# Performance work log

Measured on AMD Instinct MI355X. Metric: run time of the kernel, lower is better.

## Reference

```python
import jax, jax.numpy as jnp
import numpy as np

B, S, D = 1, 2048, 4096
H, KV, HD = 32, 8, 128
REP = H // KV            # 4, GQA repeat factor
THETA = 500000.0
NEG = -1e9               # stand-in for -inf in additive causal mask


def _rope(x, cos, sin):
    # x: [B,S,h,HD]; complex rotation on interleaved (even,odd) pairs,
    # matching torch.view_as_complex on [..., HD/2, 2]
    xr, xi = x[..., 0::2], x[..., 1::2]
    c = cos[None, :, None, :]
    s = sin[None, :, None, :]
    out_r = xr * c - xi * s
    out_i = xr * s + xi * c
    return jnp.stack([out_r, out_i], axis=-1).reshape(x.shape)


def setup_inputs() -> dict:
    key = jax.random.key(0)
    ks = jax.random.split(key, 6)
    x = jax.random.normal(ks[0], (B, S, D), dtype=jnp.float32)
    # torch nn.Linear weights are [out, in]
    sc = 1.0 / np.sqrt(D)
    wq = jax.random.normal(ks[1], (H * HD, D), dtype=jnp.float32) * sc
    wk = jax.random.normal(ks[2], (KV * HD, D), dtype=jnp.float32) * sc
    wv = jax.random.normal(ks[3], (KV * HD, D), dtype=jnp.float32) * sc
    wo = jax.random.normal(ks[4], (D, H * HD), dtype=jnp.float32) * sc
    # RoPE freqs_cis = exp(i * t * theta_f), stored as cos/sin [S, HD/2]
    freqs = 1.0 / (THETA ** (jnp.arange(0, HD, 2, dtype=jnp.float32) / HD))
    ang = jnp.outer(jnp.arange(S, dtype=jnp.float32), freqs)
    cos, sin = jnp.cos(ang), jnp.sin(ang)
    cache = jnp.zeros((2, B, S, KV, HD), dtype=jnp.float32)
    mask = jnp.where(jnp.tril(jnp.ones((S, S), dtype=bool)), 0.0, NEG).astype(jnp.float32)
    return {"x": x, "wq": wq, "wk": wk, "wv": wv, "wo": wo,
            "cos": cos, "sin": sin, "cache": cache, "mask": mask,
            "start_pos": 0}


def reference(x, wq, wk, wv, wo, cos, sin, cache, mask, start_pos):
    b, s, _ = x.shape
    xq = (x @ wq.T).reshape(b, s, H, HD)
    xk = (x @ wk.T).reshape(b, s, KV, HD)
    xv = (x @ wv.T).reshape(b, s, KV, HD)
    xq = _rope(xq, cos, sin)
    xk = _rope(xk, cos, sin)
    # functional KV-cache write
    cache = cache.at[0, :b, start_pos:start_pos + s].set(xk)
    cache = cache.at[1, :b, start_pos:start_pos + s].set(xv)
    keys = cache[0, :b, :start_pos + s]    # [b,T,KV,HD]
    values = cache[1, :b, :start_pos + s]  # [b,T,KV,HD]
    # GQA: head h = kv*REP + r (repeat_interleave ordering)
    q = xq.reshape(b, s, KV, REP, HD)
    scores = jnp.einsum('bskrd,btkd->bkrst', q, keys) / jnp.sqrt(jnp.float32(HD))
    scores = scores + mask[None, None, None]           # [b,KV,REP,s,T]
    p = jax.nn.softmax(scores.astype(jnp.float32), axis=-1).astype(x.dtype)
    out = jnp.einsum('bkrst,btkd->bskrd', p, values).reshape(b, s, H * HD)
    return out @ wo.T
```

## Files before the change

kernel.cpp:

```cpp
#include <hip/hip_runtime.h>
#include <stdint.h>

typedef __bf16 bf16_8 __attribute__((ext_vector_type(8)));
typedef __bf16 bf16_4 __attribute__((ext_vector_type(4)));
typedef float  f32x4  __attribute__((ext_vector_type(4)));

#define B_  1
#define S_  2048
#define D_  4096
#define H_  32
#define KV_ 8
#define HD_ 128

__device__ inline void gload_lds16(const void* g, void* l) {
  __builtin_amdgcn_global_load_lds((const __attribute__((address_space(1))) void*)g,
                                   (__attribute__((address_space(3))) void*)l, 16, 0, 0);
}

__global__ __launch_bounds__(256) void cvt_all(const float* __restrict__ x,
                                               const float* __restrict__ wq,
                                               const float* __restrict__ wk,
                                               const float* __restrict__ wv,
                                               const float* __restrict__ wo,
                                               __bf16* __restrict__ dst) {
  int i = blockIdx.x * 256 + threadIdx.x;
  const float* s;
  int j = i;
  if (j < 2097152) s = x;
  else if ((j -= 2097152) < 4194304) s = wq;
  else if ((j -= 4194304) < 1048576) s = wk;
  else if ((j -= 1048576) < 1048576) s = wv;
  else { j -= 1048576; s = wo; }
  float4 v = ((const float4*)s)[j];
  bf16_4 o = { (__bf16)v.x, (__bf16)v.y, (__bf16)v.z, (__bf16)v.w };
  ((bf16_4*)dst)[i] = o;
}

__global__ __launch_bounds__(256) void rope_k(__bf16* __restrict__ Qb, __bf16* __restrict__ Kb,
                                              const float* __restrict__ cosT,
                                              const float* __restrict__ sinT) {
  int t = blockIdx.x * 256 + threadIdx.x;
  const int NQ = S_ * (D_ / 8);
  __bf16* p;
  int row, cl8;
  if (t < NQ) { row = t >> 9; cl8 = t & 511; p = Qb + (size_t)row * D_ + cl8 * 8; }
  else        { int u = t - NQ; row = u >> 7; cl8 = u & 127; p = Kb + (size_t)row * 1024 + cl8 * 8; }
  bf16_8 v = *(bf16_8*)p;
  int fi0 = ((cl8 * 8) & 127) >> 1;
  float4 c4 = *(const float4*)&cosT[row * 64 + fi0];
  float4 s4 = *(const float4*)&sinT[row * 64 + fi0];
  float cc[4] = {c4.x, c4.y, c4.z, c4.w};
  float ss[4] = {s4.x, s4.y, s4.z, s4.w};
  bf16_8 o;
#pragma unroll
  for (int j = 0; j < 4; ++j) {
    float xr = (float)v[2 * j], xi = (float)v[2 * j + 1];
    o[2 * j]     = (__bf16)(xr * cc[j] - xi * ss[j]);
    o[2 * j + 1] = (__bf16)(xr * ss[j] + xi * cc[j]);
  }
  *(bf16_8*)p = o;
}


#define STAGE_A(BF, KT, BAND)                                                      \
  {                                                                                \
    int c_ = wid * 64 + lane;                                                      \
    int cs_ = c_ ^ ((c_ >> 3) & 7);                                                \
    gload_lds16(Ag + (size_t)((BAND) * 64 + (c_ >> 3)) * 4096 + (KT) * 64 + (cs_ & 7) * 8, \
                &Abuf[BF][(BAND) * 4096 + wid * 512]);                             \
  }
#define STAGE_B(BF, KT)                                                            \
  {                                                                                \
    _Pragma("unroll")                                                              \
    for (int l_ = 0; l_ < 4; ++l_) {                                               \
      int c_ = l_ * 512 + wid * 64 + lane;                                         \
      int cs_ = c_ ^ ((c_ >> 3) & 7);                                              \
      gload_lds16(Wg + (size_t)(c_ >> 3) * 4096 + (KT) * 64 + (cs_ & 7) * 8,       \
                  &Bbuf[BF][l_ * 4096 + wid * 512]);                               \
    }                                                                              \
  }
#define READ_A(P)                                                                  \
  _Pragma("unroll")                                                                \
  for (int r2 = 0; r2 < 2; ++r2)                                                   \
    _Pragma("unroll")                                                              \
    for (int ks = 0; ks < 2; ++ks) {                                               \
      int row_ = (P) * 64 + wm * 32 + r2 * 16 + (lane & 15);                       \
      int bo_ = (row_ * 128 + (ks * 32 + (lane >> 4) * 8) * 2) ^ ((row_ & 7) << 4);\
      aq[r2][ks] = *(const bf16_8*)(Ab + bo_);                                     \
    }
#define READ_B()                                                                   \
  _Pragma("unroll")                                                                \
  for (int j = 0; j < 4; ++j)                                                      \
    _Pragma("unroll")                                                              \
    for (int ks = 0; ks < 2; ++ks) {                                               \
      int row_ = wn * 64 + j * 16 + (lane & 15);                                   \
      int bo_ = (row_ * 128 + (ks * 32 + (lane >> 4) * 8) * 2) ^ ((row_ & 7) << 4);\
      bq[j][ks] = *(const bf16_8*)(Bb + bo_);                                      \
    }
#define PHASE_MFMA(P)                                                              \
  __builtin_amdgcn_s_setprio(1);                                                   \
  _Pragma("unroll")                                                                \
  for (int r2 = 0; r2 < 2; ++r2)                                                   \
    _Pragma("unroll")                                                              \
    for (int j = 0; j < 4; ++j)                                                    \
      _Pragma("unroll")                                                            \
      for (int ks = 0; ks < 2; ++ks)                                               \
        acc[P][r2][j] =                                                            \
            __builtin_amdgcn_mfma_f32_16x16x32_bf16(aq[r2][ks], bq[j][ks], acc[P][r2][j], 0, 0, 0); \
  __builtin_amdgcn_s_setprio(0);

__global__ __launch_bounds__(512) void gemm8_qkv(const __bf16* __restrict__ xb,
                                                 const __bf16* __restrict__ wqb,
                                                 const __bf16* __restrict__ wkb,
                                                 const __bf16* __restrict__ wvb,
                                                 __bf16* __restrict__ Qb,
                                                 __bf16* __restrict__ Kb,
                                                 __bf16* __restrict__ Vt) {
  __shared__ __bf16 Abuf[2][16384];
  __shared__ __bf16 Bbuf[2][16384];
  const int nb = blockIdx.x, mb = blockIdx.y;
  const int tid = threadIdx.x, lane = tid & 63, wid = tid >> 6;
  const int wm = wid >> 2, wn = wid & 3;

  const __bf16* Wg;
  if (nb < 16)      Wg = wqb + (size_t)nb * 256 * 4096;
  else if (nb < 20) Wg = wkb + (size_t)(nb - 16) * 256 * 4096;
  else              Wg = wvb + (size_t)(nb - 20) * 256 * 4096;
  const __bf16* Ag = xb + (size_t)mb * 256 * 4096;

  const f32x4 zv = {0.f, 0.f, 0.f, 0.f};
  f32x4 acc[4][2][4];
#pragma unroll
  for (int q = 0; q < 4; ++q)
#pragma unroll
    for (int r2 = 0; r2 < 2; ++r2)
#pragma unroll
      for (int j = 0; j < 4; ++j) acc[q][r2][j] = zv;

  STAGE_B(0, 0);
  STAGE_A(0, 0, 0); STAGE_A(0, 0, 1); STAGE_A(0, 0, 2); STAGE_A(0, 0, 3);
  STAGE_B(1, 1);
  STAGE_A(1, 1, 0); STAGE_A(1, 1, 1); STAGE_A(1, 1, 2);

  for (int kt = 0; kt < 64; ++kt) {
    const int cur = kt & 1;
    const char* Ab = (const char*)&Abuf[cur][0];
    const char* Bb = (const char*)&Bbuf[cur][0];
    if (kt == 63) { asm volatile("s_waitcnt vmcnt(0)" ::: "memory"); }
    else          { asm volatile("s_waitcnt vmcnt(7)" ::: "memory"); }
    __builtin_amdgcn_s_barrier();

    bf16_8 bq[4][2], aq[2][2];
    READ_B();
    READ_A(0);
    __builtin_amdgcn_s_barrier();
    asm volatile("s_waitcnt lgkmcnt(0)" ::: "memory");
    __builtin_amdgcn_sched_barrier(0);
    if (kt + 1 < 64) { STAGE_A(cur ^ 1, kt + 1, 3); }
    PHASE_MFMA(0);
    READ_A(1);
    __builtin_amdgcn_s_barrier();
    asm volatile("s_waitcnt lgkmcnt(0)" ::: "memory");
    __builtin_amdgcn_sched_barrier(0);
    if (kt + 2 < 64) { STAGE_B(cur, kt + 2); }
    PHASE_MFMA(1);
    READ_A(2);
    __builtin_amdgcn_s_barrier();
    asm volatile("s_waitcnt lgkmcnt(0)" ::: "memory");
    __builtin_amdgcn_sched_barrier(0);
    if (kt + 2 < 64) { STAGE_A(cur, kt + 2, 0); STAGE_A(cur, kt + 2, 1); }
    PHASE_MFMA(2);
    READ_A(3);
    __builtin_amdgcn_s_barrier();
    asm volatile("s_waitcnt lgkmcnt(0)" ::: "memory");
    __builtin_amdgcn_sched_barrier(0);
    if (kt + 2 < 64) { STAGE_A(cur, kt + 2, 2); }
    PHASE_MFMA(3);
  }

#pragma unroll
  for (int q = 0; q < 4; ++q)
#pragma unroll
    for (int r2 = 0; r2 < 2; ++r2)
#pragma unroll
      for (int j = 0; j < 4; ++j) {
        int rowb = mb * 256 + q * 64 + wm * 32 + r2 * 16 + (lane >> 4) * 4;
        int col = wn * 64 + j * 16 + (lane & 15);
        if (nb < 16) {
          int colg = nb * 256 + col;
#pragma unroll
          for (int r = 0; r < 4; ++r)
            Qb[(size_t)(rowb + r) * D_ + colg] = (__bf16)acc[q][r2][j][r];
        } else if (nb < 20) {
          int colg = (nb - 16) * 256 + col;
#pragma unroll
          for (int r = 0; r < 4; ++r)
            Kb[(size_t)(rowb + r) * 1024 + colg] = (__bf16)acc[q][r2][j][r];
        } else {
          int colg = (nb - 20) * 256 + col;
          bf16_4 pv = { (__bf16)acc[q][r2][j][0], (__bf16)acc[q][r2][j][1],
                        (__bf16)acc[q][r2][j][2], (__bf16)acc[q][r2][j][3] };
          *(bf16_4*)&Vt[(size_t)colg * S_ + rowb] = pv;
        }
      }
}

__global__ __launch_bounds__(256) void gemm_out(const __bf16* __restrict__ Ob,
                                                const __bf16* __restrict__ wob,
                                                float* __restrict__ Of) {
  __shared__ __bf16 As[128 * 32];
  __shared__ __bf16 Bs[128 * 32];
  const int nb = blockIdx.x, mb = blockIdx.y;
  const int tid = threadIdx.x, lane = tid & 63, wv = tid >> 6;
  const int wm = wv >> 1, wn = wv & 1;
  const int srow = lane >> 2, scol = (lane & 3) * 8;

  const __bf16* Ag0 = Ob  + (size_t)(mb * 128 + 2 * wv * 16 + srow) * D_ + scol;
  const __bf16* Bg0 = wob + (size_t)(nb * 128 + 2 * wv * 16 + srow) * D_ + scol;
  __bf16* Al = As + 2 * wv * 512;
  __bf16* Bl = Bs + 2 * wv * 512;

  const f32x4 zv = {0.f, 0.f, 0.f, 0.f};
  f32x4 acc[4][4];
#pragma unroll
  for (int i = 0; i < 4; ++i)
#pragma unroll
    for (int j = 0; j < 4; ++j) acc[i][j] = zv;

  for (int k0 = 0; k0 < D_; k0 += 32) {
    gload_lds16(Ag0 + k0, Al);
    gload_lds16(Ag0 + (size_t)16 * D_ + k0, Al + 512);
    gload_lds16(Bg0 + k0, Bl);
    gload_lds16(Bg0 + (size_t)16 * D_ + k0, Bl + 512);
    __syncthreads();
    bf16_8 af[4], bfr[4];
#pragma unroll
    for (int i = 0; i < 4; ++i)
      af[i] = *(const bf16_8*)&As[(wm * 64 + i * 16 + (lane & 15)) * 32 + (lane >> 4) * 8];
#pragma unroll
    for (int j = 0; j < 4; ++j)
      bfr[j] = *(const bf16_8*)&Bs[(wn * 64 + j * 16 + (lane & 15)) * 32 + (lane >> 4) * 8];
#pragma unroll
    for (int i = 0; i < 4; ++i)
#pragma unroll
      for (int j = 0; j < 4; ++j)
        acc[i][j] = __builtin_amdgcn_mfma_f32_16x16x32_bf16(af[i], bfr[j], acc[i][j], 0, 0, 0);
    __syncthreads();
  }

#pragma unroll
  for (int i = 0; i < 4; ++i) {
    int row0 = mb * 128 + wm * 64 + i * 16 + (lane >> 4) * 4;
#pragma unroll
    for (int j = 0; j < 4; ++j) {
      int colg = nb * 128 + wn * 64 + j * 16 + (lane & 15);
#pragma unroll
      for (int r = 0; r < 4; ++r)
        Of[(size_t)(row0 + r) * D_ + colg] = acc[i][j][r];
    }
  }
}

#define COMPUTE_TILE(ACC, MR, LR, AQ, QB0, DOMASK, KSB, VSB)                       \
  {                                                                                \
    f32x4 sfr_[4];                                                                 \
    __builtin_amdgcn_s_setprio(1);                                                 \
    _Pragma("unroll")                                                              \
    for (int nf = 0; nf < 4; ++nf) {                                               \
      f32x4 c_ = zv;                                                               \
      _Pragma("unroll")                                                            \
      for (int ks = 0; ks < 4; ++ks) {                                             \
        int n_ = nf * 16 + (lane & 15);                                            \
        int bo_ = (n_ * 256 + (ks * 32 + (lane >> 4) * 8) * 2) ^ ((n_ & 7) << 4);  \
        bf16_8 bk_ = *(const bf16_8*)((char*)(KSB) + bo_);                         \
        c_ = __builtin_amdgcn_mfma_f32_16x16x32_bf16(bk_, AQ[ks], c_, 0, 0, 0);    \
      }                                                                            \
      sfr_[nf] = c_;                                                               \
    }                                                                              \
    __builtin_amdgcn_s_setprio(0);                                                 \
    const int myq_ = (QB0) + w * 16 + (lane & 15);                                 \
    float pm_ = -3e38f;                                                            \
    _Pragma("unroll")                                                              \
    for (int nf = 0; nf < 4; ++nf) {                                               \
      _Pragma("unroll")                                                            \
      for (int r = 0; r < 4; ++r) {                                                \
        int kcol_ = kb * 64 + nf * 16 + (lane >> 4) * 4 + r;                       \
        float v_ = sfr_[nf][r] * sc;                                               \
        if ((DOMASK) && kcol_ > myq_) v_ = -1e9f;                                  \
        sfr_[nf][r] = v_;                                                          \
        pm_ = fmaxf(pm_, v_);                                                      \
      }                                                                            \
    }                                                                              \
    pm_ = fmaxf(pm_, __shfl_xor(pm_, 16));                                         \
    pm_ = fmaxf(pm_, __shfl_xor(pm_, 32));                                         \
    if (!__all(pm_ <= MR + 8.f)) {                                                 \
      float mn_ = fmaxf(MR, pm_);                                                  \
      float rs_ = __expf(MR - mn_);                                                \
      MR = mn_;                                                                    \
      LR *= rs_;                                                                   \
      float rsb_[4];                                                               \
      _Pragma("unroll")                                                            \
      for (int r = 0; r < 4; ++r)                                                  \
        rsb_[r] = __shfl(rs_, (lane & 48) | ((lane >> 4) * 4 + r));                \
      _Pragma("unroll")                                                            \
      for (int d = 0; d < 8; ++d)                                                  \
        _Pragma("unroll")                                                          \
        for (int r = 0; r < 4; ++r) ACC[d][r] *= rsb_[r];                          \
    }                                                                              \
    float ps_ = 0.f;                                                               \
    _Pragma("unroll")                                                              \
    for (int nf = 0; nf < 4; ++nf) {                                               \
      bf16_4 pk_;                                                                  \
      _Pragma("unroll")                                                            \
      for (int r = 0; r < 4; ++r) {                                                \
        float p_ = __expf(sfr_[nf][r] - MR);                                       \
        ps_ += p_;                                                                 \
        pk_[r] = (__bf16)p_;                                                       \
      }                                                                            \
      int bo_ = ((lane & 15) * 128 + nf * 32 + (lane >> 4) * 8) ^                  \
                (((lane & 15) & 7) << 4);                                          \
      *(bf16_4*)((char*)(&Ps[w][0]) + bo_) = pk_;                                  \
    }                                                                              \
    ps_ += __shfl_xor(ps_, 16);                                                    \
    ps_ += __shfl_xor(ps_, 32);                                                    \
    LR += ps_;                                                                     \
    bf16_8 ap_[2];                                                                 \
    _Pragma("unroll")                                                              \
    for (int ks = 0; ks < 2; ++ks) {                                               \
      int bo_ = ((lane & 15) * 128 + (ks * 32 + (lane >> 4) * 8) * 2) ^            \
                (((lane & 15) & 7) << 4);                                          \
      ap_[ks] = *(const bf16_8*)((char*)(&Ps[w][0]) + bo_);                        \
    }                                                                              \
    __builtin_amdgcn_s_setprio(1);                                                 \
    _Pragma("unroll")                                                              \
    for (int d = 0; d < 8; ++d) {                                                  \
      _Pragma("unroll")                                                            \
      for (int ks = 0; ks < 2; ++ks) {                                             \
        int dr_ = d * 16 + (lane & 15);                                            \
        int bo_ = (dr_ * 128 + (ks * 32 + (lane >> 4) * 8) * 2) ^ ((dr_ & 7) << 4);\
        bf16_8 bv_ = *(const bf16_8*)((char*)(VSB) + bo_);                         \
        ACC[d] = __builtin_amdgcn_mfma_f32_16x16x32_bf16(ap_[ks], bv_, ACC[d], 0, 0, 0); \
      }                                                                            \
    }                                                                              \
    __builtin_amdgcn_s_setprio(0);                                                 \
  }

__global__ __launch_bounds__(256) void attn_k(const __bf16* __restrict__ Qb,
                                              const __bf16* __restrict__ Kb,
                                              const __bf16* __restrict__ Vt,
                                              __bf16* __restrict__ Ob) {
  __shared__ __bf16 Ks[2][64 * 128];
  __shared__ __bf16 Vs[2][128 * 64];
  __shared__ __bf16 Ps[4][16 * 64];
  const int x = blockIdx.x, h = blockIdx.y, kvh = h >> 2;
  const int qlo = x, qhi = 31 - x;
  const int tid = threadIdx.x, lane = tid & 63, w = tid >> 6;

  bf16_8 aq0[4], aq1[4];
#pragma unroll
  for (int ks = 0; ks < 4; ++ks) {
    int rr = w * 16 + (lane & 15);
    int cc = h * 128 + ks * 32 + (lane >> 4) * 8;
    aq0[ks] = *(const bf16_8*)&Qb[(size_t)(qlo * 64 + rr) * D_ + cc];
    aq1[ks] = *(const bf16_8*)&Qb[(size_t)(qhi * 64 + rr) * D_ + cc];
  }

  const f32x4 zv = {0.f, 0.f, 0.f, 0.f};
  f32x4 accO0[8], accO1[8];
#pragma unroll
  for (int d = 0; d < 8; ++d) { accO0[d] = zv; accO1[d] = zv; }
  float mr0 = -3e38f, lr0 = 0.f, mr1 = -3e38f, lr1 = 0.f;

  const float sc = 0.08838834764831845f;

  bf16_8 rK[4], rV[4];
#define KLOAD(KB)                                                                  \
  {                                                                                \
    _Pragma("unroll")                                                              \
    for (int u = 0; u < 4; ++u) {                                                  \
      int cid = u * 256 + tid; int row = cid >> 4, c8 = cid & 15;                  \
      rK[u] = *(const bf16_8*)&Kb[(size_t)((KB) * 64 + row) * 1024 + kvh * 128 + c8 * 8]; \
    }                                                                              \
    _Pragma("unroll")                                                              \
    for (int u = 0; u < 4; ++u) {                                                  \
      int cid = u * 256 + tid; int vr = cid >> 3, c8 = cid & 7;                    \
      rV[u] = *(const bf16_8*)&Vt[(size_t)(kvh * 128 + vr) * S_ + (KB) * 64 + c8 * 8]; \
    }                                                                              \
  }
#define KSTORE(BUF)                                                                \
  {                                                                                \
    _Pragma("unroll")                                                              \
    for (int u = 0; u < 4; ++u) {                                                  \
      int cid = u * 256 + tid; int row = cid >> 4, c8 = cid & 15;                  \
      int bo = (row * 256 + c8 * 16) ^ ((row & 7) << 4);                           \
      *(bf16_8*)((char*)(&Ks[BUF][0]) + bo) = rK[u];                               \
    }                                                                              \
    _Pragma("unroll")                                                              \
    for (int u = 0; u < 4; ++u) {                                                  \
      int cid = u * 256 + tid; int vr = cid >> 3, c8 = cid & 7;                    \
      int bo = (vr * 128 + c8 * 16) ^ ((vr & 7) << 4);                             \
      *(bf16_8*)((char*)(&Vs[BUF][0]) + bo) = rV[u];                               \
    }                                                                              \
  }

  KLOAD(0);
  KSTORE(0);
  __syncthreads();

  for (int kb = 0; kb <= qhi; ++kb) {
    const int cur = kb & 1;
    if (kb < qhi) KLOAD(kb + 1);
    __bf16* ksb = &Ks[cur][0];
    __bf16* vsb = &Vs[cur][0];
    COMPUTE_TILE(accO1, mr1, lr1, aq1, qhi * 64, (kb == qhi), ksb, vsb);
    if (kb <= qlo) COMPUTE_TILE(accO0, mr0, lr0, aq0, qlo * 64, (kb == qlo), ksb, vsb);
    if (kb < qhi) {
      KSTORE(cur ^ 1);
      __syncthreads();
    }
  }

  float inv0[4], inv1[4];
#pragma unroll
  for (int r = 0; r < 4; ++r) {
    int src = (lane & 48) | ((lane >> 4) * 4 + r);
    inv0[r] = 1.0f / __shfl(lr0, src);
    inv1[r] = 1.0f / __shfl(lr1, src);
  }
#pragma unroll
  for (int d = 0; d < 8; ++d) {
#pragma unroll
    for (int r = 0; r < 4; ++r) {
      size_t rl = (size_t)(qlo * 64 + w * 16 + (lane >> 4) * 4 + r);
      size_t rh = (size_t)(qhi * 64 + w * 16 + (lane >> 4) * 4 + r);
      int cc = h * 128 + d * 16 + (lane & 15);
      Ob[rl * D_ + cc] = (__bf16)(accO0[d][r] * inv0[r]);
      Ob[rh * D_ + cc] = (__bf16)(accO1[d][r] * inv1[r]);
    }
  }
}

extern "C" void kernel_launch(void* const* d_in, const int* in_sizes, int n_in,
                              void* d_out, int out_size, void* d_ws, size_t ws_size,
                              hipStream_t stream) {
  const float* x    = (const float*)d_in[0];
  const float* wq   = (const float*)d_in[1];
  const float* wk   = (const float*)d_in[2];
  const float* wv   = (const float*)d_in[3];
  const float* wo   = (const float*)d_in[4];
  const float* cosT = (const float*)d_in[5];
  const float* sinT = (const float*)d_in[6];
  float* out = (float*)d_out;
  char* ws = (char*)d_ws;

  __bf16* xb  = (__bf16*)(ws + 0);
  __bf16* wqb = (__bf16*)(ws + 16777216);
  __bf16* wkb = (__bf16*)(ws + 50331648);
  __bf16* wvb = (__bf16*)(ws + 58720256);
  __bf16* wob = (__bf16*)(ws + 67108864);
  __bf16* Qb  = (__bf16*)(ws + 100663296);
  __bf16* Kb  = (__bf16*)(ws + 117440512);
  __bf16* Vt  = (__bf16*)(ws + 121634816);
  __bf16* Ob  = xb;

  cvt_all<<<49152, 256, 0, stream>>>(x, wq, wk, wv, wo, xb);

  gemm8_qkv<<<dim3(24, 8), 512, 0, stream>>>(xb, wqb, wkb, wvb, Qb, Kb, Vt);

  rope_k<<<5120, 256, 0, stream>>>(Qb, Kb, cosT, sinT);

  attn_k<<<dim3(16, 32), 256, 0, stream>>>(Qb, Kb, Vt, Ob);

  gemm_out<<<dim3(32, 16), 256, 0, stream>>>(Ob, wob, out);
}
```

Baseline: 398.7 us.

## Restage QKV GEMM prefetch per phase and use direct LDS loads in attention

The QKV GEMM pipeline is restructured so the next k-tile's B halves and A bands are issued into the other buffer across the four MFMA phases, each phase ending with a counted vmcnt wait and a barrier. The attention kernel now stages K/V tiles with global_load_lds straight into swizzled shared memory instead of going through registers, which frees registers and removes the LDS store step. The softmax scale is folded into Q once at load time, and the max and sum reductions are split into independent partial chains. The risks are a pipeline that is only one tile deep instead of two, extra barriers in the GEMM, and small rounding changes from scaling Q in bf16.

```diff
diff --git a/kernel.cpp b/kernel.cpp
--- a/kernel.cpp
+++ b/kernel.cpp
@@ -61,7 +61,6 @@
   *(bf16_8*)p = o;
 }
 
-
 #define STAGE_A(BF, KT, BAND)                                                      \
   {                                                                                \
     int c_ = wid * 64 + lane;                                                      \
@@ -69,10 +68,10 @@
     gload_lds16(Ag + (size_t)((BAND) * 64 + (c_ >> 3)) * 4096 + (KT) * 64 + (cs_ & 7) * 8, \
                 &Abuf[BF][(BAND) * 4096 + wid * 512]);                             \
   }
-#define STAGE_B(BF, KT)                                                            \
+#define STAGE_BH(BF, KT, HF)                                                       \
   {                                                                                \
     _Pragma("unroll")                                                              \
-    for (int l_ = 0; l_ < 4; ++l_) {                                               \
+    for (int l_ = 2 * (HF); l_ < 2 * (HF) + 2; ++l_) {                             \
       int c_ = l_ * 512 + wid * 64 + lane;                                         \
       int cs_ = c_ ^ ((c_ >> 3) & 7);                                              \
       gload_lds16(Wg + (size_t)(c_ >> 3) * 4096 + (KT) * 64 + (cs_ & 7) * 8,       \
@@ -108,6 +107,13 @@
         acc[P][r2][j] =                                                            \
             __builtin_amdgcn_mfma_f32_16x16x32_bf16(aq[r2][ks], bq[j][ks], acc[P][r2][j], 0, 0, 0); \
   __builtin_amdgcn_s_setprio(0);
+#define PH_PRE()                                                                   \
+  __builtin_amdgcn_s_barrier();                                                    \
+  asm volatile("s_waitcnt lgkmcnt(0)" ::: "memory");                               \
+  __builtin_amdgcn_sched_barrier(0);
+#define PH_POST(N)                                                                 \
+  asm volatile("s_waitcnt vmcnt(" #N ")" ::: "memory");                            \
+  __builtin_amdgcn_s_barrier();
 
 __global__ __launch_bounds__(512) void gemm8_qkv(const __bf16* __restrict__ xb,
                                                  const __bf16* __restrict__ wqb,
@@ -137,45 +143,38 @@
 #pragma unroll
       for (int j = 0; j < 4; ++j) acc[q][r2][j] = zv;
 
-  STAGE_B(0, 0);
+  STAGE_BH(0, 0, 0); STAGE_BH(0, 0, 1);
   STAGE_A(0, 0, 0); STAGE_A(0, 0, 1); STAGE_A(0, 0, 2); STAGE_A(0, 0, 3);
-  STAGE_B(1, 1);
-  STAGE_A(1, 1, 0); STAGE_A(1, 1, 1); STAGE_A(1, 1, 2);
-
-  for (int kt = 0; kt < 64; ++kt) {
-    const int cur = kt & 1;
+  asm volatile("s_waitcnt vmcnt(3)" ::: "memory");
+  __builtin_amdgcn_s_barrier();
+
+  for (int t = 0; t < 64; ++t) {
+    const int cur = t & 1, nxt = cur ^ 1;
+    const bool so = (t < 63);
     const char* Ab = (const char*)&Abuf[cur][0];
     const char* Bb = (const char*)&Bbuf[cur][0];
-    if (kt == 63) { asm volatile("s_waitcnt vmcnt(0)" ::: "memory"); }
-    else          { asm volatile("s_waitcnt vmcnt(7)" ::: "memory"); }
-    __builtin_amdgcn_s_barrier();
-
     bf16_8 bq[4][2], aq[2][2];
     READ_B();
     READ_A(0);
-    __builtin_amdgcn_s_barrier();
-    asm volatile("s_waitcnt lgkmcnt(0)" ::: "memory");
-    __builtin_amdgcn_sched_barrier(0);
-    if (kt + 1 < 64) { STAGE_A(cur ^ 1, kt + 1, 3); }
+    if (so) { STAGE_BH(nxt, t + 1, 0); }
+    PH_PRE();
     PHASE_MFMA(0);
+    PH_POST(4);
     READ_A(1);
-    __builtin_amdgcn_s_barrier();
-    asm volatile("s_waitcnt lgkmcnt(0)" ::: "memory");
-    __builtin_amdgcn_sched_barrier(0);
-    if (kt + 2 < 64) { STAGE_B(cur, kt + 2); }
+    if (so) { STAGE_BH(nxt, t + 1, 1); }
+    PH_PRE();
     PHASE_MFMA(1);
+    PH_POST(5);
     READ_A(2);
-    __builtin_amdgcn_s_barrier();
-    asm volatile("s_waitcnt lgkmcnt(0)" ::: "memory");
-    __builtin_amdgcn_sched_barrier(0);
-    if (kt + 2 < 64) { STAGE_A(cur, kt + 2, 0); STAGE_A(cur, kt + 2, 1); }
+    if (so) { STAGE_A(nxt, t + 1, 0); STAGE_A(nxt, t + 1, 1); }
+    PH_PRE();
     PHASE_MFMA(2);
+    PH_POST(6);
     READ_A(3);
-    __builtin_amdgcn_s_barrier();
-    asm volatile("s_waitcnt lgkmcnt(0)" ::: "memory");
-    __builtin_amdgcn_sched_barrier(0);
-    if (kt + 2 < 64) { STAGE_A(cur, kt + 2, 2); }
+    if (so) { STAGE_A(nxt, t + 1, 2); STAGE_A(nxt, t + 1, 3); }
+    PH_PRE();
     PHASE_MFMA(3);
+    PH_POST(3);
   }
 
 #pragma unroll
@@ -279,18 +278,21 @@
     }                                                                              \
     __builtin_amdgcn_s_setprio(0);                                                 \
     const int myq_ = (QB0) + w * 16 + (lane & 15);                                 \
-    float pm_ = -3e38f;                                                            \
+    float pmn_[4];                                                                 \
     _Pragma("unroll")                                                              \
     for (int nf = 0; nf < 4; ++nf) {                                               \
+      float t_ = -3e38f;                                                           \
       _Pragma("unroll")                                                            \
       for (int r = 0; r < 4; ++r) {                                                \
         int kcol_ = kb * 64 + nf * 16 + (lane >> 4) * 4 + r;                       \
-        float v_ = sfr_[nf][r] * sc;                                               \
+        float v_ = sfr_[nf][r];                                                    \
         if ((DOMASK) && kcol_ > myq_) v_ = -1e9f;                                  \
         sfr_[nf][r] = v_;                                                          \
-        pm_ = fmaxf(pm_, v_);                                                      \
+        t_ = fmaxf(t_, v_);                                                        \
       }                                                                            \
-    }                                                                              \
+      pmn_[nf] = t_;                                                               \
+    }                                                                              \
+    float pm_ = fmaxf(fmaxf(pmn_[0], pmn_[1]), fmaxf(pmn_[2], pmn_[3]));           \
     pm_ = fmaxf(pm_, __shfl_xor(pm_, 16));                                         \
     pm_ = fmaxf(pm_, __shfl_xor(pm_, 32));                                         \
     if (!__all(pm_ <= MR + 8.f)) {                                                 \
@@ -307,20 +309,23 @@
         _Pragma("unroll")                                                          \
         for (int r = 0; r < 4; ++r) ACC[d][r] *= rsb_[r];                          \
     }                                                                              \
-    float ps_ = 0.f;                                                               \
+    float psn_[4];                                                                 \
     _Pragma("unroll")                                                              \
     for (int nf = 0; nf < 4; ++nf) {                                               \
       bf16_4 pk_;                                                                  \
+      float t_ = 0.f;                                                              \
       _Pragma("unroll")                                                            \
       for (int r = 0; r < 4; ++r) {                                                \
         float p_ = __expf(sfr_[nf][r] - MR);                                       \
-        ps_ += p_;                                                                 \
+        t_ += p_;                                                                  \
         pk_[r] = (__bf16)p_;                                                       \
       }                                                                            \
+      psn_[nf] = t_;                                                               \
       int bo_ = ((lane & 15) * 128 + nf * 32 + (lane >> 4) * 8) ^                  \
                 (((lane & 15) & 7) << 4);                                          \
       *(bf16_4*)((char*)(&Ps[w][0]) + bo_) = pk_;                                  \
     }                                                                              \
+    float ps_ = (psn_[0] + psn_[1]) + (psn_[2] + psn_[3]);                         \
     ps_ += __shfl_xor(ps_, 16);                                                    \
     ps_ += __shfl_xor(ps_, 32);                                                    \
     LR += ps_;                                                                     \
@@ -356,13 +361,20 @@
   const int qlo = x, qhi = 31 - x;
   const int tid = threadIdx.x, lane = tid & 63, w = tid >> 6;
 
+  const float sc = 0.08838834764831845f;
+
   bf16_8 aq0[4], aq1[4];
 #pragma unroll
   for (int ks = 0; ks < 4; ++ks) {
     int rr = w * 16 + (lane & 15);
     int cc = h * 128 + ks * 32 + (lane >> 4) * 8;
-    aq0[ks] = *(const bf16_8*)&Qb[(size_t)(qlo * 64 + rr) * D_ + cc];
-    aq1[ks] = *(const bf16_8*)&Qb[(size_t)(qhi * 64 + rr) * D_ + cc];
+    bf16_8 t0 = *(const bf16_8*)&Qb[(size_t)(qlo * 64 + rr) * D_ + cc];
+    bf16_8 t1 = *(const bf16_8*)&Qb[(size_t)(qhi * 64 + rr) * D_ + cc];
+#pragma unroll
+    for (int e = 0; e < 8; ++e) {
+      aq0[ks][e] = (__bf16)((float)t0[e] * sc);
+      aq1[ks][e] = (__bf16)((float)t1[e] * sc);
+    }
   }
 
   const f32x4 zv = {0.f, 0.f, 0.f, 0.f};
@@ -371,51 +383,37 @@
   for (int d = 0; d < 8; ++d) { accO0[d] = zv; accO1[d] = zv; }
   float mr0 = -3e38f, lr0 = 0.f, mr1 = -3e38f, lr1 = 0.f;
 
-  const float sc = 0.08838834764831845f;
-
-  bf16_8 rK[4], rV[4];
-#define KLOAD(KB)                                                                  \
+#define KSTAGE(BUF, KB)                                                            \
   {                                                                                \
     _Pragma("unroll")                                                              \
     for (int u = 0; u < 4; ++u) {                                                  \
-      int cid = u * 256 + tid; int row = cid >> 4, c8 = cid & 15;                  \
-      rK[u] = *(const bf16_8*)&Kb[(size_t)((KB) * 64 + row) * 1024 + kvh * 128 + c8 * 8]; \
+      int chunk = (u * 4 + w) * 64 + lane;                                         \
+      int row = chunk >> 4, p8 = chunk & 15;                                       \
+      gload_lds16(&Kb[(size_t)((KB) * 64 + row) * 1024 + kvh * 128 + (p8 ^ (row & 7)) * 8], \
+                  &Ks[BUF][(u * 4 + w) * 512]);                                    \
     }                                                                              \
     _Pragma("unroll")                                                              \
     for (int u = 0; u < 4; ++u) {                                                  \
-      int cid = u * 256 + tid; int vr = cid >> 3, c8 = cid & 7;                    \
-      rV[u] = *(const bf16_8*)&Vt[(size_t)(kvh * 128 + vr) * S_ + (KB) * 64 + c8 * 8]; \
-    }                                                                              \
-  }
-#define KSTORE(BUF)                                                                \
-  {                                                                                \
-    _Pragma("unroll")                                                              \
-    for (int u = 0; u < 4; ++u) {                                                  \
-      int cid = u * 256 + tid; int row = cid >> 4, c8 = cid & 15;                  \
-      int bo = (row * 256 + c8 * 16) ^ ((row & 7) << 4);                           \
-      *(bf16_8*)((char*)(&Ks[BUF][0]) + bo) = rK[u];                               \
-    }                                                                              \
-    _Pragma("unroll")                                                              \
-    for (int u = 0; u < 4; ++u) {                                                  \
-      int cid = u * 256 + tid; int vr = cid >> 3, c8 = cid & 7;                    \
-      int bo = (vr * 128 + c8 * 16) ^ ((vr & 7) << 4);                             \
-      *(bf16_8*)((char*)(&Vs[BUF][0]) + bo) = rV[u];                               \
-    }                                                                              \
-  }
-
-  KLOAD(0);
-  KSTORE(0);
+      int chunk = (u * 4 + w) * 64 + lane;                                         \
+      int vr = chunk >> 3, p8 = chunk & 7;                                         \
+      gload_lds16(&Vt[(size_t)(kvh * 128 + vr) * S_ + (KB) * 64 + (p8 ^ (vr & 7)) * 8], \
+                  &Vs[BUF][(u * 4 + w) * 512]);                                    \
+    }                                                                              \
+  }
+
+  KSTAGE(0, 0);
+  asm volatile("s_waitcnt vmcnt(0)" ::: "memory");
   __syncthreads();
 
   for (int kb = 0; kb <= qhi; ++kb) {
     const int cur = kb & 1;
-    if (kb < qhi) KLOAD(kb + 1);
-    __bf16* ksb = &Ks[cur][0];
-    __bf16* vsb = &Vs[cur][0];
+    if (kb < qhi) KSTAGE(cur ^ 1, kb + 1);
+    const __bf16* ksb = &Ks[cur][0];
+    const __bf16* vsb = &Vs[cur][0];
     COMPUTE_TILE(accO1, mr1, lr1, aq1, qhi * 64, (kb == qhi), ksb, vsb);
     if (kb <= qlo) COMPUTE_TILE(accO0, mr0, lr0, aq0, qlo * 64, (kb == qlo), ksb, vsb);
     if (kb < qhi) {
-      KSTORE(cur ^ 1);
+      asm volatile("s_waitcnt vmcnt(0)" ::: "memory");
       __syncthreads();
     }
   }
```

New measurement: 382.2 us. 1.04x faster.
